# Performance work log

Hardware: AMD Instinct MI355X
Metric: run time of the kernel (lower is better)

Reference implementation:

```python
import jax, jax.numpy as jnp
import numpy as np

N = 1024       # sample size
ZC = 64        # z_c dim
ZD = 64        # z_d dim
H = ZC         # FF hidden dim = zc_dim per InfoNCE.__init__


def setup_inputs() -> dict:
    key = jax.random.key(0)
    ks = jax.random.split(key, 6)
    s1 = 1.0 / np.sqrt(ZC + ZD)
    s2 = 1.0 / np.sqrt(H)
    return {
        "z_c": jax.random.normal(ks[0], (N, ZC), jnp.float32),
        "z_d": jax.random.normal(ks[1], (N, ZD), jnp.float32),
        # FF params: Linear(ZC+ZD,H) -> relu -> Linear(H,H) -> relu -> Linear(H,1)
        "W1": jax.random.normal(ks[2], (ZC + ZD, H), jnp.float32) * s1,
        "b1": jnp.zeros((H,), jnp.float32),
        "W2": jax.random.normal(ks[3], (H, H), jnp.float32) * s2,
        "b2": jnp.zeros((H,), jnp.float32),
        "Wo": jax.random.normal(ks[4], (H, 1), jnp.float32) * s2,
        "bo": jnp.zeros((1,), jnp.float32),
    }


def reference(z_c, z_d, W1, b1, W2, b2, Wo, bo):
    n = z_d.shape[0]
    zc_dim = z_c.shape[-1]

    # T0: critic on matched pairs, input concat([z_c, z_d]) -> [N, 1]
    x0 = jnp.concatenate([z_c, z_d], axis=-1)
    h0 = jax.nn.relu(x0 @ W1 + b1)
    h0 = jax.nn.relu(h0 @ W2 + b2)
    T0 = h0 @ Wo + bo  # [N, 1]

    # T1: critic on all NxN pairs. Instead of materializing the tiled
    # concat [N, N, ZC+ZD], decompose the first linear layer:
    # concat([zc_tile, zd_tile]) @ W1 == zc_tile @ W1c + zd_tile @ W1d.
    # zc_tile[i, j] = z_c[j], zd_tile[i, j] = z_d[i]  (exact same math).
    W1c, W1d = W1[:zc_dim], W1[zc_dim:]
    h1 = jax.nn.relu((z_c @ W1c)[None, :, :] + (z_d @ W1d)[:, None, :] + b1)  # [N, N, H]
    h2 = jax.nn.relu(h1 @ W2 + b2)                                            # [N, N, H]
    T1 = (h2 @ Wo + bo)[..., 0]                                               # [N, N]

    lower_bound = T0.mean() - (jax.nn.logsumexp(T1, axis=1).mean() - jnp.log(jnp.float32(n)))
    return lower_bound
```

## Files before the change

kernel.cpp:

```cpp
#include <hip/hip_runtime.h>
#include <hip/hip_fp16.h>
#include <math.h>

#define NN 1024

typedef _Float16 half8 __attribute__((ext_vector_type(8)));
typedef float f32x4 __attribute__((ext_vector_type(4)));

union H8U { uint4 u; half8 h; };

__device__ __forceinline__ unsigned short h_bits(float x) {
    _Float16 h = (_Float16)x;
    unsigned short b;
    __builtin_memcpy(&b, &h, 2);
    return b;
}

__global__ void prep_kernel(const float* __restrict__ z_c, const float* __restrict__ z_d,
                            const float* __restrict__ W1, const float* __restrict__ b1,
                            const float* __restrict__ W2,
                            unsigned short* __restrict__ Aph,
                            unsigned short* __restrict__ Bph,
                            uint4* __restrict__ W2h) {
    if (blockIdx.x < 512) {
        int t = blockIdx.x * 256 + threadIdx.x;
        int sel = t >> 16;
        int idx = t & 0xffff;
        int n = idx >> 6, h = idx & 63;
        const float* z = (sel ? z_d : z_c) + n * 64;
        const float* w = W1 + (sel ? 4096 : 0) + h;
        float a0 = sel ? 0.f : b1[h], a1 = 0.f;
        #pragma unroll
        for (int k = 0; k < 64; k += 2) {
            a0 = fmaf(z[k],     w[k * 64],       a0);
            a1 = fmaf(z[k + 1], w[(k + 1) * 64], a1);
        }
        unsigned short val = h_bits(a0 + a1);
        int s = h >> 5, q = (h >> 3) & 3, e = h & 7;
        if (sel) {
            Bph[n * 64 + q * 16 + s * 8 + e] = val;
        } else {
            Aph[(n >> 4) * 1024 + (q * 16 + (n & 15)) * 16 + s * 8 + e] = val;
        }
    } else {
        int tt = (blockIdx.x - 512) * 256 + threadIdx.x;
        int f = tt >> 6, lane = tt & 63;
        int s = f >> 2, t4 = f & 3, q = lane >> 4, l15 = lane & 15;
        int n = t4 * 16 + l15;
        unsigned w4[4];
        #pragma unroll
        for (int p = 0; p < 4; ++p) {
            int k = s * 32 + q * 8 + 2 * p;
            unsigned lo = h_bits(W2[k * 64 + n]);
            unsigned hi = h_bits(W2[(k + 1) * 64 + n]);
            w4[p] = lo | (hi << 16);
        }
        W2h[f * 64 + lane] = make_uint4(w4[0], w4[1], w4[2], w4[3]);
    }
}

__global__ void __launch_bounds__(256, 4)
main_kernel(const unsigned short* __restrict__ Aph, const unsigned short* __restrict__ Bph,
            const uint4* __restrict__ W2h,
            const float* __restrict__ b2, const float* __restrict__ Wo,
            float* __restrict__ Crow) {
    const int i    = blockIdx.x;
    const int rot  = blockIdx.x & 15;
    const int tid  = threadIdx.x;
    const int lane = tid & 63;
    const int wave = tid >> 6;
    const int l15  = lane & 15;
    const int q    = lane >> 4;

    __shared__ uint4 sW[512];
    __shared__ float sb2[64];
    __shared__ float sWo[64];
    __shared__ float sS[4];
    __shared__ float sT0;

    sW[tid]       = W2h[tid];
    sW[tid + 256] = W2h[tid + 256];
    if (tid < 64)                  sb2[tid]      = b2[tid];
    else if (tid < 128)            sWo[tid - 64] = Wo[tid - 64];
    __syncthreads();

    half8 W[2][4];
    #pragma unroll
    for (int f = 0; f < 8; ++f) {
        H8U u; u.u = sW[f * 64 + lane];
        W[f >> 2][f & 3] = u.h;
    }

    H8U cb0, cb1;
    {
        const uint4* bp = (const uint4*)(Bph + i * 64 + q * 16);
        cb0.u = bp[0];
        cb1.u = bp[1];
    }

    f32x4 b2v[4];
    float wov[4][4];
    #pragma unroll
    for (int t = 0; t < 4; ++t) {
        float4 bt = *(const float4*)(sb2 + t * 16 + q * 4);
        float4 wt = *(const float4*)(sWo + t * 16 + q * 4);
        b2v[t] = (f32x4){bt.x, bt.y, bt.z, bt.w};
        wov[t][0] = wt.x; wov[t][1] = wt.y; wov[t][2] = wt.z; wov[t][3] = wt.w;
    }

    const half8 zero = {0, 0, 0, 0, 0, 0, 0, 0};
    float sacc = 0.f;

    const unsigned short* ap = Aph + (wave * 16) * 1024 + lane * 16;

    H8U xa0, xa1, xb0, xb1;
    {
        const uint4* p0 = (const uint4*)(ap + ((0 + rot) & 15) * 1024);
        xa0.u = p0[0];
        xa1.u = p0[1];
        const uint4* p1 = (const uint4*)(ap + ((1 + rot) & 15) * 1024);
        xb0.u = p1[0];
        xb1.u = p1[1];
    }

    #pragma unroll
    for (int t = 0; t < 16; t += 2) {
        {
            half8 a0 = __builtin_elementwise_max(xa0.h + cb0.h, zero);
            half8 a1 = __builtin_elementwise_max(xa1.h + cb1.h, zero);
            if (t + 2 < 16) {
                const uint4* nx = (const uint4*)(ap + ((t + 2 + rot) & 15) * 1024);
                xa0.u = nx[0];
                xa1.u = nx[1];
            }

            f32x4 acc[4];
            #pragma unroll
            for (int u = 0; u < 4; ++u) acc[u] = b2v[u];
            #pragma unroll
            for (int u = 0; u < 4; ++u) {
                acc[u] = __builtin_amdgcn_mfma_f32_16x16x32_f16(W[0][u], a0, acc[u], 0, 0, 0);
                acc[u] = __builtin_amdgcn_mfma_f32_16x16x32_f16(W[1][u], a1, acc[u], 0, 0, 0);
            }

            float p0 = 0.f, p1 = 0.f, p2 = 0.f, p3 = 0.f;
            #pragma unroll
            for (int u = 0; u < 4; ++u) {
                p0 = fmaf(fmaxf(acc[u][0], 0.f), wov[u][0], p0);
                p1 = fmaf(fmaxf(acc[u][1], 0.f), wov[u][1], p1);
                p2 = fmaf(fmaxf(acc[u][2], 0.f), wov[u][2], p2);
                p3 = fmaf(fmaxf(acc[u][3], 0.f), wov[u][3], p3);
            }
            float ps = (p0 + p1) + (p2 + p3);
            ps += __shfl_xor(ps, 16);
            ps += __shfl_xor(ps, 32);
            const int j = (wave * 16 + ((t + rot) & 15)) * 16 + l15;
            if (j == i && q == 0) sT0 = ps;
            sacc += __expf(ps);
        }
        {
            half8 a0 = __builtin_elementwise_max(xb0.h + cb0.h, zero);
            half8 a1 = __builtin_elementwise_max(xb1.h + cb1.h, zero);
            if (t + 3 < 16) {
                const uint4* nx = (const uint4*)(ap + ((t + 3 + rot) & 15) * 1024);
                xb0.u = nx[0];
                xb1.u = nx[1];
            }

            f32x4 acc[4];
            #pragma unroll
            for (int u = 0; u < 4; ++u) acc[u] = b2v[u];
            #pragma unroll
            for (int u = 0; u < 4; ++u) {
                acc[u] = __builtin_amdgcn_mfma_f32_16x16x32_f16(W[0][u], a0, acc[u], 0, 0, 0);
                acc[u] = __builtin_amdgcn_mfma_f32_16x16x32_f16(W[1][u], a1, acc[u], 0, 0, 0);
            }

            float p0 = 0.f, p1 = 0.f, p2 = 0.f, p3 = 0.f;
            #pragma unroll
            for (int u = 0; u < 4; ++u) {
                p0 = fmaf(fmaxf(acc[u][0], 0.f), wov[u][0], p0);
                p1 = fmaf(fmaxf(acc[u][1], 0.f), wov[u][1], p1);
                p2 = fmaf(fmaxf(acc[u][2], 0.f), wov[u][2], p2);
                p3 = fmaf(fmaxf(acc[u][3], 0.f), wov[u][3], p3);
            }
            float ps = (p0 + p1) + (p2 + p3);
            ps += __shfl_xor(ps, 16);
            ps += __shfl_xor(ps, 32);
            const int j = (wave * 16 + ((t + 1 + rot) & 15)) * 16 + l15;
            if (j == i && q == 0) sT0 = ps;
            sacc += __expf(ps);
        }
    }

    sacc += __shfl_xor(sacc, 1);
    sacc += __shfl_xor(sacc, 2);
    sacc += __shfl_xor(sacc, 4);
    sacc += __shfl_xor(sacc, 8);
    if (lane == 0) sS[wave] = sacc;
    __syncthreads();
    if (tid == 0) {
        float S = (sS[0] + sS[1]) + (sS[2] + sS[3]);
        Crow[i] = sT0 - logf(S);
    }
}

__global__ void __launch_bounds__(1024)
combine_finish(const float* __restrict__ Crow, float* __restrict__ out) {
    float c = Crow[threadIdx.x];
    #pragma unroll
    for (int off = 1; off < 64; off <<= 1) c += __shfl_xor(c, off);
    __shared__ float sc[16];
    int w = threadIdx.x >> 6;
    if ((threadIdx.x & 63) == 0) sc[w] = c;
    __syncthreads();
    if (threadIdx.x == 0) {
        float C = 0.f;
        #pragma unroll
        for (int k = 0; k < 16; ++k) C += sc[k];
        out[0] = C * (1.0f / 1024.0f) + 6.9314718055994531f;
    }
}

extern "C" void kernel_launch(void* const* d_in, const int* in_sizes, int n_in,
                              void* d_out, int out_size, void* d_ws, size_t ws_size,
                              hipStream_t stream) {
    const float* z_c = (const float*)d_in[0];
    const float* z_d = (const float*)d_in[1];
    const float* W1  = (const float*)d_in[2];
    const float* b1  = (const float*)d_in[3];
    const float* W2  = (const float*)d_in[4];
    const float* b2  = (const float*)d_in[5];
    const float* Wo  = (const float*)d_in[6];
    float* out   = (float*)d_out;

    unsigned short* Aph = (unsigned short*)d_ws;
    unsigned short* Bph = Aph + NN * 64;
    uint4* W2h   = (uint4*)(Bph + NN * 64);
    float* Crow  = (float*)(W2h + 512);

    prep_kernel<<<514, 256, 0, stream>>>(z_c, z_d, W1, b1, W2, Aph, Bph, W2h);
    main_kernel<<<1024, 256, 0, stream>>>(Aph, Bph, W2h, b2, Wo, Crow);
    combine_finish<<<1, 1024, 0, stream>>>(Crow, out);
}
```

Measured before the change: 84.57 us.

## Split each row across two blocks and read W2 fragments from LDS

Each row i of the NxN critic is now processed by two blocks, each covering half the columns, so the grid doubles to 2048 blocks. Partial exp-sums and the diagonal T0 value go to global memory and are combined in the finish kernel. W2 fragments are read from LDS inside the MFMA loop instead of being held in registers, and launch bounds are raised to 5 blocks per SIMD. The aim is more parallelism, higher occupancy and a shorter per-block tail, at the cost of duplicated per-block setup (the W2 copy into LDS) and extra LDS reads in the inner loop.

```diff
diff --git a/kernel.cpp b/kernel.cpp
--- a/kernel.cpp
+++ b/kernel.cpp
@@ -59,13 +59,15 @@
     }
 }
 
-__global__ void __launch_bounds__(256, 4)
+__global__ void __launch_bounds__(256, 5)
 main_kernel(const unsigned short* __restrict__ Aph, const unsigned short* __restrict__ Bph,
             const uint4* __restrict__ W2h,
             const float* __restrict__ b2, const float* __restrict__ Wo,
-            float* __restrict__ Crow) {
-    const int i    = blockIdx.x;
-    const int rot  = blockIdx.x & 15;
+            float* __restrict__ Shalf, float* __restrict__ T0row) {
+    const int bid  = blockIdx.x;
+    const int i    = bid >> 1;
+    const int hh   = bid & 1;
+    const int rot  = bid & 7;
     const int tid  = threadIdx.x;
     const int lane = tid & 63;
     const int wave = tid >> 6;
@@ -76,20 +78,12 @@
     __shared__ float sb2[64];
     __shared__ float sWo[64];
     __shared__ float sS[4];
-    __shared__ float sT0;
 
     sW[tid]       = W2h[tid];
     sW[tid + 256] = W2h[tid + 256];
     if (tid < 64)                  sb2[tid]      = b2[tid];
     else if (tid < 128)            sWo[tid - 64] = Wo[tid - 64];
     __syncthreads();
-
-    half8 W[2][4];
-    #pragma unroll
-    for (int f = 0; f < 8; ++f) {
-        H8U u; u.u = sW[f * 64 + lane];
-        W[f >> 2][f & 3] = u.h;
-    }
 
     H8U cb0, cb1;
     {
@@ -111,25 +105,26 @@
     const half8 zero = {0, 0, 0, 0, 0, 0, 0, 0};
     float sacc = 0.f;
 
-    const unsigned short* ap = Aph + (wave * 16) * 1024 + lane * 16;
+    const int tbase = hh * 32 + wave * 8;
+    const unsigned short* ap = Aph + tbase * 1024 + lane * 16;
 
     H8U xa0, xa1, xb0, xb1;
     {
-        const uint4* p0 = (const uint4*)(ap + ((0 + rot) & 15) * 1024);
+        const uint4* p0 = (const uint4*)(ap + ((0 + rot) & 7) * 1024);
         xa0.u = p0[0];
         xa1.u = p0[1];
-        const uint4* p1 = (const uint4*)(ap + ((1 + rot) & 15) * 1024);
+        const uint4* p1 = (const uint4*)(ap + ((1 + rot) & 7) * 1024);
         xb0.u = p1[0];
         xb1.u = p1[1];
     }
 
     #pragma unroll
-    for (int t = 0; t < 16; t += 2) {
+    for (int t = 0; t < 8; t += 2) {
         {
             half8 a0 = __builtin_elementwise_max(xa0.h + cb0.h, zero);
             half8 a1 = __builtin_elementwise_max(xa1.h + cb1.h, zero);
-            if (t + 2 < 16) {
-                const uint4* nx = (const uint4*)(ap + ((t + 2 + rot) & 15) * 1024);
+            if (t + 2 < 8) {
+                const uint4* nx = (const uint4*)(ap + ((t + 2 + rot) & 7) * 1024);
                 xa0.u = nx[0];
                 xa1.u = nx[1];
             }
@@ -139,8 +134,10 @@
             for (int u = 0; u < 4; ++u) acc[u] = b2v[u];
             #pragma unroll
             for (int u = 0; u < 4; ++u) {
-                acc[u] = __builtin_amdgcn_mfma_f32_16x16x32_f16(W[0][u], a0, acc[u], 0, 0, 0);
-                acc[u] = __builtin_amdgcn_mfma_f32_16x16x32_f16(W[1][u], a1, acc[u], 0, 0, 0);
+                H8U w0; w0.u = sW[u * 64 + lane];
+                acc[u] = __builtin_amdgcn_mfma_f32_16x16x32_f16(w0.h, a0, acc[u], 0, 0, 0);
+                H8U w1; w1.u = sW[(4 + u) * 64 + lane];
+                acc[u] = __builtin_amdgcn_mfma_f32_16x16x32_f16(w1.h, a1, acc[u], 0, 0, 0);
             }
 
             float p0 = 0.f, p1 = 0.f, p2 = 0.f, p3 = 0.f;
@@ -154,15 +151,15 @@
             float ps = (p0 + p1) + (p2 + p3);
             ps += __shfl_xor(ps, 16);
             ps += __shfl_xor(ps, 32);
-            const int j = (wave * 16 + ((t + rot) & 15)) * 16 + l15;
-            if (j == i && q == 0) sT0 = ps;
+            const int j = (tbase + ((t + rot) & 7)) * 16 + l15;
+            if (j == i && q == 0) T0row[i] = ps;
             sacc += __expf(ps);
         }
         {
             half8 a0 = __builtin_elementwise_max(xb0.h + cb0.h, zero);
             half8 a1 = __builtin_elementwise_max(xb1.h + cb1.h, zero);
-            if (t + 3 < 16) {
-                const uint4* nx = (const uint4*)(ap + ((t + 3 + rot) & 15) * 1024);
+            if (t + 3 < 8) {
+                const uint4* nx = (const uint4*)(ap + ((t + 3 + rot) & 7) * 1024);
                 xb0.u = nx[0];
                 xb1.u = nx[1];
             }
@@ -172,8 +169,10 @@
             for (int u = 0; u < 4; ++u) acc[u] = b2v[u];
             #pragma unroll
             for (int u = 0; u < 4; ++u) {
-                acc[u] = __builtin_amdgcn_mfma_f32_16x16x32_f16(W[0][u], a0, acc[u], 0, 0, 0);
-                acc[u] = __builtin_amdgcn_mfma_f32_16x16x32_f16(W[1][u], a1, acc[u], 0, 0, 0);
+                H8U w0; w0.u = sW[u * 64 + lane];
+                acc[u] = __builtin_amdgcn_mfma_f32_16x16x32_f16(w0.h, a0, acc[u], 0, 0, 0);
+                H8U w1; w1.u = sW[(4 + u) * 64 + lane];
+                acc[u] = __builtin_amdgcn_mfma_f32_16x16x32_f16(w1.h, a1, acc[u], 0, 0, 0);
             }
 
             float p0 = 0.f, p1 = 0.f, p2 = 0.f, p3 = 0.f;
@@ -187,8 +186,8 @@
             float ps = (p0 + p1) + (p2 + p3);
             ps += __shfl_xor(ps, 16);
             ps += __shfl_xor(ps, 32);
-            const int j = (wave * 16 + ((t + 1 + rot) & 15)) * 16 + l15;
-            if (j == i && q == 0) sT0 = ps;
+            const int j = (tbase + ((t + 1 + rot) & 7)) * 16 + l15;
+            if (j == i && q == 0) T0row[i] = ps;
             sacc += __expf(ps);
         }
     }
@@ -199,15 +198,16 @@
     sacc += __shfl_xor(sacc, 8);
     if (lane == 0) sS[wave] = sacc;
     __syncthreads();
-    if (tid == 0) {
-        float S = (sS[0] + sS[1]) + (sS[2] + sS[3]);
-        Crow[i] = sT0 - logf(S);
-    }
+    if (tid == 0)
+        Shalf[bid] = (sS[0] + sS[1]) + (sS[2] + sS[3]);
 }
 
 __global__ void __launch_bounds__(1024)
-combine_finish(const float* __restrict__ Crow, float* __restrict__ out) {
-    float c = Crow[threadIdx.x];
+combine_finish(const float* __restrict__ Shalf, const float* __restrict__ T0row,
+               float* __restrict__ out) {
+    int i = threadIdx.x;
+    float S = Shalf[2 * i] + Shalf[2 * i + 1];
+    float c = T0row[i] - logf(S);
     #pragma unroll
     for (int off = 1; off < 64; off <<= 1) c += __shfl_xor(c, off);
     __shared__ float sc[16];
@@ -237,9 +237,10 @@
     unsigned short* Aph = (unsigned short*)d_ws;
     unsigned short* Bph = Aph + NN * 64;
     uint4* W2h   = (uint4*)(Bph + NN * 64);
-    float* Crow  = (float*)(W2h + 512);
+    float* Shalf = (float*)(W2h + 512);
+    float* T0row = Shalf + 2 * NN;
 
     prep_kernel<<<514, 256, 0, stream>>>(z_c, z_d, W1, b1, W2, Aph, Bph, W2h);
-    main_kernel<<<1024, 256, 0, stream>>>(Aph, Bph, W2h, b2, Wo, Crow);
-    combine_finish<<<1, 1024, 0, stream>>>(Crow, out);
-}
+    main_kernel<<<2048, 256, 0, stream>>>(Aph, Bph, W2h, b2, Wo, Shalf, T0row);
+    combine_finish<<<1, 1024, 0, stream>>>(Shalf, T0row, out);
+}
```

New measurement: 158.3 us. 1.87x slower.
